# Optimization experiments

Measured on AMD Instinct MI355X. Metric: run time of the kernel, lower is better.

Reference implementation:

```python
import jax, jax.numpy as jnp
import numpy as np

MIN_PTS = 4

def setup_inputs() -> dict:
    key = jax.random.key(0)
    ks = jax.random.split(key, 10)
    P, N = 2048, 256            # proposals, max points per proposal slot
    H1, H2, OUT = 64, 128, 256  # PointNet MLP widths, extractor out_dim
    points = jax.random.normal(ks[0], (P, N, 3), dtype=jnp.float32)
    lengths = jax.random.randint(ks[1], (P,), 0, N, dtype=jnp.int32)  # some < MIN_PTS -> invalid
    centers = jax.random.normal(ks[2], (P, 3), dtype=jnp.float32) * 10.0
    sizes = jax.random.uniform(ks[3], (P, 3), minval=0.5, maxval=4.0, dtype=jnp.float32)
    proposals = jnp.concatenate([centers, sizes], axis=1)  # (P, 6)
    def lin(k, fan_in, fan_out):
        return jax.random.normal(k, (fan_in, fan_out), dtype=jnp.float32) * np.float32(1.0 / np.sqrt(fan_in))
    return {
        'points': points, 'lengths': lengths, 'proposals': proposals,
        'W1': lin(ks[4], 3, H1),   'b1': jnp.zeros((H1,), jnp.float32),
        'W2': lin(ks[5], H1, H2),  'b2': jnp.zeros((H2,), jnp.float32),
        'W3': lin(ks[6], H2, OUT), 'b3': jnp.zeros((OUT,), jnp.float32),
        'Wc': lin(ks[7], OUT, 1),  'bc': jnp.zeros((1,), jnp.float32),
        'Wr': lin(ks[8], OUT, 4),  'br': jnp.zeros((4,), jnp.float32),
    }

def reference(points, lengths, proposals, W1, b1, W2, b2, W3, b3, Wc, bc, Wr, br):
    P, N, _ = points.shape
    # repeat-padding: point i of proposal p maps to index i % n_p (gather form of the torch loop)
    L = jnp.maximum(lengths, 1)
    idx = jnp.arange(N, dtype=lengths.dtype)[None, :] % L[:, None]          # (P, N)
    batched = jnp.take_along_axis(points, idx[:, :, None], axis=1)         # (P, N, 3)
    # MultiPositionExtractor: box-normalized coords -> pointwise MLP -> max-pool
    centers = proposals[:, :3]
    half = proposals[:, 3:] * 0.5 + 1e-6
    local = (batched - centers[:, None, :]) / half[:, None, :]             # (P, N, 3)
    h = jax.nn.relu(local @ W1 + b1)                                       # (P, N, 64)
    h = jax.nn.relu(h @ W2 + b2)                                           # (P, N, 128)
    h = jax.nn.relu(h @ W3 + b3)                                           # (P, N, 256)
    feats = jnp.max(h, axis=1)                                             # (P, 256)
    # scatter-back: proposals with < MIN_PTS points get zero feature vector
    valid = lengths >= MIN_PTS
    feats = jnp.where(valid[:, None], feats, jnp.zeros((), feats.dtype))
    cls_logits = feats @ Wc + bc                                           # (P, 1)
    reg_deltas = feats @ Wr + br                                           # (P, 4)
    return cls_logits, reg_deltas
```

## Files before the change

kernel.cpp:

```cpp
#include <hip/hip_runtime.h>

#define MIN_PTS 4

typedef short bf16x8 __attribute__((ext_vector_type(8)));
typedef float f32x4  __attribute__((ext_vector_type(4)));

__device__ __forceinline__ ushort f2bf(float x) {
    unsigned u = __float_as_uint(x);
    u = (u + 0x7fffu + ((u >> 16) & 1u)) >> 16;
    return (ushort)u;
}

__global__ void pack_weights(const float* __restrict__ W2, const float* __restrict__ W3,
                             ushort* __restrict__ B2P, ushort* __restrict__ B3P)
{
    int idx = blockIdx.x * 256 + threadIdx.x;
    if (idx < 8192) {
        int j = idx & 7, l = (idx >> 3) & 63, ks = (idx >> 9) & 1, nt = idx >> 10;
        int k   = ks * 32 + (l >> 4) * 8 + j;
        int col = nt * 16 + (l & 15);
        B2P[idx] = f2bf(W2[k * 128 + col]);
    }
    if (idx < 32768) {
        int j = idx & 7, l = (idx >> 3) & 63, ks = (idx >> 9) & 3, nt = idx >> 11;
        int k   = ks * 32 + (l >> 4) * 8 + j;
        int col = nt * 16 + (l & 15);
        B3P[idx] = f2bf(W3[k * 256 + col]);
    }
}

__global__ __launch_bounds__(512, 8) void refine_stripe(
    const float* __restrict__ points,
    const int*   __restrict__ lengths,
    const float* __restrict__ proposals,
    const float* __restrict__ W1, const float* __restrict__ b1,
    const float* __restrict__ b2,
    const float* __restrict__ b3,
    const ushort* __restrict__ B2P, const ushort* __restrict__ B3P,
    int* __restrict__ featsG,
    int P, int N)
{
    const int p   = blockIdx.x;
    const int s   = blockIdx.y;
    const int len = lengths[p];
    if (len < MIN_PTS || s * 64 >= len) return;

    __shared__ __align__(16) ushort A1[4096];
    __shared__ __align__(16) ushort A3[8192];

    const int tid  = threadIdx.x;
    const int lane = tid & 63;
    const int w    = tid >> 6;
    const int rc   = lane & 15;
    const int g    = lane >> 4;

    const float cx = proposals[p * 6 + 0];
    const float cy = proposals[p * 6 + 1];
    const float cz = proposals[p * 6 + 2];
    const float rhx = __builtin_amdgcn_rcpf(fmaf(proposals[p * 6 + 3], 0.5f, 1e-6f));
    const float rhy = __builtin_amdgcn_rcpf(fmaf(proposals[p * 6 + 4], 0.5f, 1e-6f));
    const float rhz = __builtin_amdgcn_rcpf(fmaf(proposals[p * 6 + 5], 0.5f, 1e-6f));

    {
        const int jj = min(s * 64 + lane, len - 1);
        const float* pt = points + (p * N + jj) * 3;
        const float x0 = (pt[0] - cx) * rhx;
        const float x1 = (pt[1] - cy) * rhy;
        const float x2 = (pt[2] - cz) * rhz;

        union { ushort u[8]; uint4 q; } t;
        #pragma unroll
        for (int i = 0; i < 8; ++i) {
            const int f = w * 8 + i;
            float v = fmaf(x0, W1[f], fmaf(x1, W1[64 + f], fmaf(x2, W1[128 + f], b1[f])));
            t.u[i] = f2bf(fmaxf(v, 0.f));
        }
        const int mt = lane >> 4, r = lane & 15;
        const int chunk = (mt * 2 + (w >> 2)) * 64 + (w & 3) * 16 + r;
        *(uint4*)&A1[chunk * 8] = t.q;
    }
    __syncthreads();

    {
        f32x4 acc2[4];
        #pragma unroll
        for (int mt = 0; mt < 4; ++mt) acc2[mt] = (f32x4){0.f, 0.f, 0.f, 0.f};

        #pragma unroll
        for (int ks = 0; ks < 2; ++ks) {
            const bf16x8 bw = *(const bf16x8*)(B2P + ((w * 2 + ks) * 64 + lane) * 8);
            #pragma unroll
            for (int mt = 0; mt < 4; ++mt) {
                const bf16x8 a = *(const bf16x8*)&A1[((mt * 2 + ks) * 64 + lane) * 8];
                acc2[mt] = __builtin_amdgcn_mfma_f32_16x16x32_bf16(bw, a, acc2[mt], 0, 0, 0);
            }
        }
        float bias2v[4];
        #pragma unroll
        for (int rr = 0; rr < 4; ++rr) bias2v[rr] = b2[16 * w + 4 * g + rr];

        const int ks3 = w >> 1;
        const int g3  = (2 * w + (g >> 1)) & 3;
        #pragma unroll
        for (int mt = 0; mt < 4; ++mt) {
            const uint u0 = (uint)f2bf(fmaxf(acc2[mt][0] + bias2v[0], 0.f))
                          | ((uint)f2bf(fmaxf(acc2[mt][1] + bias2v[1], 0.f)) << 16);
            const uint u1 = (uint)f2bf(fmaxf(acc2[mt][2] + bias2v[2], 0.f))
                          | ((uint)f2bf(fmaxf(acc2[mt][3] + bias2v[3], 0.f)) << 16);
            const int chunk = (mt * 4 + ks3) * 64 + g3 * 16 + rc;
            uint2 val; val.x = u0; val.y = u1;
            *(uint2*)&A3[chunk * 8 + (g & 1) * 4] = val;
        }
    }
    __syncthreads();

    {
        f32x4 acc3[4][2];
        #pragma unroll
        for (int mt = 0; mt < 4; ++mt)
            #pragma unroll
            for (int j = 0; j < 2; ++j)
                acc3[mt][j] = (f32x4){0.f, 0.f, 0.f, 0.f};

        #pragma unroll
        for (int ks = 0; ks < 4; ++ks) {
            const bf16x8 bf0 = *(const bf16x8*)(B3P + (((2 * w + 0) * 4 + ks) * 64 + lane) * 8);
            const bf16x8 bf1 = *(const bf16x8*)(B3P + (((2 * w + 1) * 4 + ks) * 64 + lane) * 8);
            #pragma unroll
            for (int mt = 0; mt < 4; ++mt) {
                const bf16x8 a = *(const bf16x8*)&A3[((mt * 4 + ks) * 64 + lane) * 8];
                acc3[mt][0] = __builtin_amdgcn_mfma_f32_16x16x32_bf16(a, bf0, acc3[mt][0], 0, 0, 0);
                acc3[mt][1] = __builtin_amdgcn_mfma_f32_16x16x32_bf16(a, bf1, acc3[mt][1], 0, 0, 0);
            }
        }

        float pool[2];
        #pragma unroll
        for (int j = 0; j < 2; ++j) {
            const float b3v = b3[16 * (2 * w + j) + rc];
            float m = 0.f;
            #pragma unroll
            for (int mt = 0; mt < 4; ++mt)
                #pragma unroll
                for (int rr = 0; rr < 4; ++rr)
                    m = fmaxf(m, acc3[mt][j][rr] + b3v);
            pool[j] = m;
        }
        #pragma unroll
        for (int j = 0; j < 2; ++j) {
            pool[j] = fmaxf(pool[j], __shfl_xor(pool[j], 16, 64));
            pool[j] = fmaxf(pool[j], __shfl_xor(pool[j], 32, 64));
        }
        if (g == 0) {
            #pragma unroll
            for (int j = 0; j < 2; ++j)
                atomicMax(&featsG[p * 256 + (2 * w + j) * 16 + rc], __float_as_int(pool[j]));
        }
    }
}

__global__ __launch_bounds__(256) void heads_kernel(
    const int* __restrict__ featsG,
    const float* __restrict__ Wc, const float* __restrict__ bc,
    const float* __restrict__ Wr, const float* __restrict__ br,
    float* __restrict__ out, int P)
{
    const int tid  = threadIdx.x;
    const int lane = tid & 63;
    const int p    = blockIdx.x * 4 + (tid >> 6);
    if (p >= P) return;

    const int4 vi = *(const int4*)&featsG[p * 256 + lane * 4];
    float v[4] = {__int_as_float(vi.x), __int_as_float(vi.y),
                  __int_as_float(vi.z), __int_as_float(vi.w)};

    const float4 wc = *(const float4*)&Wc[lane * 4];
    float c  = v[0] * wc.x + v[1] * wc.y + v[2] * wc.z + v[3] * wc.w;
    float r0 = 0.f, r1 = 0.f, r2 = 0.f, r3 = 0.f;
    #pragma unroll
    for (int i = 0; i < 4; ++i) {
        const float4 wr = *(const float4*)&Wr[(lane * 4 + i) * 4];
        r0 = fmaf(v[i], wr.x, r0);
        r1 = fmaf(v[i], wr.y, r1);
        r2 = fmaf(v[i], wr.z, r2);
        r3 = fmaf(v[i], wr.w, r3);
    }
    #pragma unroll
    for (int off = 32; off > 0; off >>= 1) {
        c  += __shfl_xor(c,  off, 64);
        r0 += __shfl_xor(r0, off, 64);
        r1 += __shfl_xor(r1, off, 64);
        r2 += __shfl_xor(r2, off, 64);
        r3 += __shfl_xor(r3, off, 64);
    }
    if (lane == 0) {
        out[p]             = c  + bc[0];
        out[P + p * 4 + 0] = r0 + br[0];
        out[P + p * 4 + 1] = r1 + br[1];
        out[P + p * 4 + 2] = r2 + br[2];
        out[P + p * 4 + 3] = r3 + br[3];
    }
}

extern "C" void kernel_launch(void* const* d_in, const int* in_sizes, int n_in,
                              void* d_out, int out_size, void* d_ws, size_t ws_size,
                              hipStream_t stream)
{
    const float* points    = (const float*)d_in[0];
    const int*   lengths   = (const int*)  d_in[1];
    const float* proposals = (const float*)d_in[2];
    const float* W1 = (const float*)d_in[3];
    const float* b1 = (const float*)d_in[4];
    const float* W2 = (const float*)d_in[5];
    const float* b2 = (const float*)d_in[6];
    const float* W3 = (const float*)d_in[7];
    const float* b3 = (const float*)d_in[8];
    const float* Wc = (const float*)d_in[9];
    const float* bc = (const float*)d_in[10];
    const float* Wr = (const float*)d_in[11];
    const float* br = (const float*)d_in[12];
    float* out = (float*)d_out;

    const int P = in_sizes[1];
    const int N = in_sizes[0] / (3 * P);
    const int SMAX = (N + 63) / 64;

    ushort* B2P    = (ushort*)d_ws;
    ushort* B3P    = B2P + 8192;
    int*    featsG = (int*)((char*)d_ws + 81920);

    hipMemsetAsync(featsG, 0, (size_t)P * 256 * sizeof(int), stream);
    pack_weights<<<dim3(128), dim3(256), 0, stream>>>(W2, W3, B2P, B3P);
    refine_stripe<<<dim3(P, SMAX), dim3(512), 0, stream>>>(
        points, lengths, proposals, W1, b1, b2, b3, B2P, B3P, featsG, P, N);
    heads_kernel<<<dim3((P + 3) / 4), dim3(256), 0, stream>>>(
        featsG, Wc, bc, Wr, br, out, P);
}
```

Measured before the change: 50.04 us.

## Convert stripe kernel to persistent loop with next-item prefetch and hoisted weights

Replaces the one-block-per-(proposal, stripe) grid with a persistent grid of 2048 blocks. Each block strides over work items and prefetches the next item's length, proposal box and point while the current one computes. W1, b1, the bias vectors and the layer-2 B fragments are loaded into registers once per block, biases are folded into the accumulator init, and bf16 packing uses a packed hardware conversion. This removes per-block setup and launch cost and hides global-load latency, at the cost of more register pressure and a work index that assumes four stripes per proposal.

```diff
diff --git a/kernel.cpp b/kernel.cpp
--- a/kernel.cpp
+++ b/kernel.cpp
@@ -1,4 +1,5 @@
 #include <hip/hip_runtime.h>
+#include <hip/hip_bf16.h>
 
 #define MIN_PTS 4
 
@@ -9,6 +10,12 @@
     unsigned u = __float_as_uint(x);
     u = (u + 0x7fffu + ((u >> 16) & 1u)) >> 16;
     return (ushort)u;
+}
+
+__device__ __forceinline__ uint cvt_pk_bf16(float lo, float hi) {
+    union { __hip_bfloat162 h; uint u; } cv;
+    cv.h = __float22bfloat162_rn(make_float2(lo, hi));
+    return cv.u;
 }
 
 __global__ void pack_weights(const float* __restrict__ W2, const float* __restrict__ W3,
@@ -29,7 +36,7 @@
     }
 }
 
-__global__ __launch_bounds__(512, 8) void refine_stripe(
+__global__ __launch_bounds__(512, 8) void refine_loop(
     const float* __restrict__ points,
     const int*   __restrict__ lengths,
     const float* __restrict__ proposals,
@@ -38,124 +45,149 @@
     const float* __restrict__ b3,
     const ushort* __restrict__ B2P, const ushort* __restrict__ B3P,
     int* __restrict__ featsG,
-    int P, int N)
-{
-    const int p   = blockIdx.x;
-    const int s   = blockIdx.y;
-    const int len = lengths[p];
-    if (len < MIN_PTS || s * 64 >= len) return;
-
+    int P, int N, int work, int NB)
+{
     __shared__ __align__(16) ushort A1[4096];
     __shared__ __align__(16) ushort A3[8192];
 
     const int tid  = threadIdx.x;
     const int lane = tid & 63;
-    const int w    = tid >> 6;
+    const int wu   = __builtin_amdgcn_readfirstlane(tid >> 6);
     const int rc   = lane & 15;
     const int g    = lane >> 4;
 
-    const float cx = proposals[p * 6 + 0];
-    const float cy = proposals[p * 6 + 1];
-    const float cz = proposals[p * 6 + 2];
-    const float rhx = __builtin_amdgcn_rcpf(fmaf(proposals[p * 6 + 3], 0.5f, 1e-6f));
-    const float rhy = __builtin_amdgcn_rcpf(fmaf(proposals[p * 6 + 4], 0.5f, 1e-6f));
-    const float rhz = __builtin_amdgcn_rcpf(fmaf(proposals[p * 6 + 5], 0.5f, 1e-6f));
-
+    float w1a[8], w1b[8], w1c[8], b1r[8];
+    #pragma unroll
+    for (int i = 0; i < 8; ++i) {
+        const int f = wu * 8 + i;
+        w1a[i] = W1[f]; w1b[i] = W1[64 + f]; w1c[i] = W1[128 + f]; b1r[i] = b1[f];
+    }
+    f32x4 bias2q;
+    #pragma unroll
+    for (int rr = 0; rr < 4; ++rr) bias2q[rr] = b2[16 * wu + 4 * g + rr];
+    const float b3v0 = b3[16 * (2 * wu + 0) + rc];
+    const float b3v1 = b3[16 * (2 * wu + 1) + rc];
+    bf16x8 bw2[2];
+    #pragma unroll
+    for (int ks = 0; ks < 2; ++ks)
+        bw2[ks] = *(const bf16x8*)(B2P + ((wu * 2 + ks) * 64 + lane) * 8);
+
+    ushort* const a1wr = &A1[(((lane >> 4) * 2 + (wu >> 2)) * 64 + (wu & 3) * 16 + rc) * 8];
+    const int ks3 = wu >> 1;
+    const int g3  = (2 * wu + (g >> 1)) & 3;
+
+    int q = blockIdx.x;
+    int   lenC;
+    float cxC, cyC, czC, rxC, ryC, rzC, p0C, p1C, p2C;
     {
-        const int jj = min(s * 64 + lane, len - 1);
-        const float* pt = points + (p * N + jj) * 3;
-        const float x0 = (pt[0] - cx) * rhx;
-        const float x1 = (pt[1] - cy) * rhy;
-        const float x2 = (pt[2] - cz) * rhz;
-
-        union { ushort u[8]; uint4 q; } t;
-        #pragma unroll
-        for (int i = 0; i < 8; ++i) {
-            const int f = w * 8 + i;
-            float v = fmaf(x0, W1[f], fmaf(x1, W1[64 + f], fmaf(x2, W1[128 + f], b1[f])));
-            t.u[i] = f2bf(fmaxf(v, 0.f));
+        const int pp = q >> 2, ss = q & 3;
+        lenC = lengths[pp];
+        cxC = proposals[pp * 6 + 0]; cyC = proposals[pp * 6 + 1]; czC = proposals[pp * 6 + 2];
+        rxC = __builtin_amdgcn_rcpf(fmaf(proposals[pp * 6 + 3], 0.5f, 1e-6f));
+        ryC = __builtin_amdgcn_rcpf(fmaf(proposals[pp * 6 + 4], 0.5f, 1e-6f));
+        rzC = __builtin_amdgcn_rcpf(fmaf(proposals[pp * 6 + 5], 0.5f, 1e-6f));
+        const int jj = min(ss * 64 + lane, max(lenC, 1) - 1);
+        const float* pt = points + ((long)pp * N + jj) * 3;
+        p0C = pt[0]; p1C = pt[1]; p2C = pt[2];
+    }
+
+    while (q < work) {
+        const int   pcur = q >> 2;
+        const bool  active = (lenC >= MIN_PTS) && ((q & 3) * 64 < lenC);
+        const float cx = cxC, cy = cyC, cz = czC, rx = rxC, ry = ryC, rz = rzC;
+        const float p0 = p0C, p1 = p1C, p2 = p2C;
+
+        const int qn = q + NB;
+        if (qn < work) {
+            const int pp = qn >> 2, ss = qn & 3;
+            lenC = lengths[pp];
+            cxC = proposals[pp * 6 + 0]; cyC = proposals[pp * 6 + 1]; czC = proposals[pp * 6 + 2];
+            rxC = __builtin_amdgcn_rcpf(fmaf(proposals[pp * 6 + 3], 0.5f, 1e-6f));
+            ryC = __builtin_amdgcn_rcpf(fmaf(proposals[pp * 6 + 4], 0.5f, 1e-6f));
+            rzC = __builtin_amdgcn_rcpf(fmaf(proposals[pp * 6 + 5], 0.5f, 1e-6f));
+            const int jj = min(ss * 64 + lane, max(lenC, 1) - 1);
+            const float* pt = points + ((long)pp * N + jj) * 3;
+            p0C = pt[0]; p1C = pt[1]; p2C = pt[2];
         }
-        const int mt = lane >> 4, r = lane & 15;
-        const int chunk = (mt * 2 + (w >> 2)) * 64 + (w & 3) * 16 + r;
-        *(uint4*)&A1[chunk * 8] = t.q;
-    }
-    __syncthreads();
-
-    {
-        f32x4 acc2[4];
-        #pragma unroll
-        for (int mt = 0; mt < 4; ++mt) acc2[mt] = (f32x4){0.f, 0.f, 0.f, 0.f};
-
-        #pragma unroll
-        for (int ks = 0; ks < 2; ++ks) {
-            const bf16x8 bw = *(const bf16x8*)(B2P + ((w * 2 + ks) * 64 + lane) * 8);
-            #pragma unroll
-            for (int mt = 0; mt < 4; ++mt) {
-                const bf16x8 a = *(const bf16x8*)&A1[((mt * 2 + ks) * 64 + lane) * 8];
-                acc2[mt] = __builtin_amdgcn_mfma_f32_16x16x32_bf16(bw, a, acc2[mt], 0, 0, 0);
+
+        if (active) {
+            {
+                const float x0 = (p0 - cx) * rx;
+                const float x1 = (p1 - cy) * ry;
+                const float x2 = (p2 - cz) * rz;
+                float v[8];
+                #pragma unroll
+                for (int i = 0; i < 8; ++i)
+                    v[i] = fmaxf(fmaf(x0, w1a[i], fmaf(x1, w1b[i], fmaf(x2, w1c[i], b1r[i]))), 0.f);
+                uint4 qq;
+                qq.x = cvt_pk_bf16(v[0], v[1]);
+                qq.y = cvt_pk_bf16(v[2], v[3]);
+                qq.z = cvt_pk_bf16(v[4], v[5]);
+                qq.w = cvt_pk_bf16(v[6], v[7]);
+                *(uint4*)a1wr = qq;
+            }
+            __syncthreads();
+
+            {
+                f32x4 acc2[4];
+                #pragma unroll
+                for (int mt = 0; mt < 4; ++mt) acc2[mt] = bias2q;
+
+                #pragma unroll
+                for (int ks = 0; ks < 2; ++ks)
+                    #pragma unroll
+                    for (int mt = 0; mt < 4; ++mt) {
+                        const bf16x8 a = *(const bf16x8*)&A1[((mt * 2 + ks) * 64 + lane) * 8];
+                        acc2[mt] = __builtin_amdgcn_mfma_f32_16x16x32_bf16(bw2[ks], a, acc2[mt], 0, 0, 0);
+                    }
+                #pragma unroll
+                for (int mt = 0; mt < 4; ++mt) {
+                    const uint u0 = cvt_pk_bf16(fmaxf(acc2[mt][0], 0.f), fmaxf(acc2[mt][1], 0.f));
+                    const uint u1 = cvt_pk_bf16(fmaxf(acc2[mt][2], 0.f), fmaxf(acc2[mt][3], 0.f));
+                    const int chunk = (mt * 4 + ks3) * 64 + g3 * 16 + rc;
+                    uint2 val; val.x = u0; val.y = u1;
+                    *(uint2*)&A3[chunk * 8 + (g & 1) * 4] = val;
+                }
+            }
+            __syncthreads();
+
+            {
+                f32x4 acc3a[4], acc3b[4];
+                #pragma unroll
+                for (int mt = 0; mt < 4; ++mt) {
+                    acc3a[mt] = (f32x4){b3v0, b3v0, b3v0, b3v0};
+                    acc3b[mt] = (f32x4){b3v1, b3v1, b3v1, b3v1};
+                }
+                #pragma unroll
+                for (int ks = 0; ks < 4; ++ks) {
+                    const bf16x8 bf0 = *(const bf16x8*)(B3P + (((2 * wu + 0) * 4 + ks) * 64 + lane) * 8);
+                    const bf16x8 bf1 = *(const bf16x8*)(B3P + (((2 * wu + 1) * 4 + ks) * 64 + lane) * 8);
+                    #pragma unroll
+                    for (int mt = 0; mt < 4; ++mt) {
+                        const bf16x8 a = *(const bf16x8*)&A3[((mt * 4 + ks) * 64 + lane) * 8];
+                        acc3a[mt] = __builtin_amdgcn_mfma_f32_16x16x32_bf16(a, bf0, acc3a[mt], 0, 0, 0);
+                        acc3b[mt] = __builtin_amdgcn_mfma_f32_16x16x32_bf16(a, bf1, acc3b[mt], 0, 0, 0);
+                    }
+                }
+                float pool0 = 0.f, pool1 = 0.f;
+                #pragma unroll
+                for (int mt = 0; mt < 4; ++mt)
+                    #pragma unroll
+                    for (int rr = 0; rr < 4; ++rr) {
+                        pool0 = fmaxf(pool0, acc3a[mt][rr]);
+                        pool1 = fmaxf(pool1, acc3b[mt][rr]);
+                    }
+                pool0 = fmaxf(pool0, __shfl_xor(pool0, 16, 64));
+                pool0 = fmaxf(pool0, __shfl_xor(pool0, 32, 64));
+                pool1 = fmaxf(pool1, __shfl_xor(pool1, 16, 64));
+                pool1 = fmaxf(pool1, __shfl_xor(pool1, 32, 64));
+                if (g == 0) {
+                    atomicMax(&featsG[pcur * 256 + (2 * wu + 0) * 16 + rc], __float_as_int(pool0));
+                    atomicMax(&featsG[pcur * 256 + (2 * wu + 1) * 16 + rc], __float_as_int(pool1));
+                }
             }
         }
-        float bias2v[4];
-        #pragma unroll
-        for (int rr = 0; rr < 4; ++rr) bias2v[rr] = b2[16 * w + 4 * g + rr];
-
-        const int ks3 = w >> 1;
-        const int g3  = (2 * w + (g >> 1)) & 3;
-        #pragma unroll
-        for (int mt = 0; mt < 4; ++mt) {
-            const uint u0 = (uint)f2bf(fmaxf(acc2[mt][0] + bias2v[0], 0.f))
-                          | ((uint)f2bf(fmaxf(acc2[mt][1] + bias2v[1], 0.f)) << 16);
-            const uint u1 = (uint)f2bf(fmaxf(acc2[mt][2] + bias2v[2], 0.f))
-                          | ((uint)f2bf(fmaxf(acc2[mt][3] + bias2v[3], 0.f)) << 16);
-            const int chunk = (mt * 4 + ks3) * 64 + g3 * 16 + rc;
-            uint2 val; val.x = u0; val.y = u1;
-            *(uint2*)&A3[chunk * 8 + (g & 1) * 4] = val;
-        }
-    }
-    __syncthreads();
-
-    {
-        f32x4 acc3[4][2];
-        #pragma unroll
-        for (int mt = 0; mt < 4; ++mt)
-            #pragma unroll
-            for (int j = 0; j < 2; ++j)
-                acc3[mt][j] = (f32x4){0.f, 0.f, 0.f, 0.f};
-
-        #pragma unroll
-        for (int ks = 0; ks < 4; ++ks) {
-            const bf16x8 bf0 = *(const bf16x8*)(B3P + (((2 * w + 0) * 4 + ks) * 64 + lane) * 8);
-            const bf16x8 bf1 = *(const bf16x8*)(B3P + (((2 * w + 1) * 4 + ks) * 64 + lane) * 8);
-            #pragma unroll
-            for (int mt = 0; mt < 4; ++mt) {
-                const bf16x8 a = *(const bf16x8*)&A3[((mt * 4 + ks) * 64 + lane) * 8];
-                acc3[mt][0] = __builtin_amdgcn_mfma_f32_16x16x32_bf16(a, bf0, acc3[mt][0], 0, 0, 0);
-                acc3[mt][1] = __builtin_amdgcn_mfma_f32_16x16x32_bf16(a, bf1, acc3[mt][1], 0, 0, 0);
-            }
-        }
-
-        float pool[2];
-        #pragma unroll
-        for (int j = 0; j < 2; ++j) {
-            const float b3v = b3[16 * (2 * w + j) + rc];
-            float m = 0.f;
-            #pragma unroll
-            for (int mt = 0; mt < 4; ++mt)
-                #pragma unroll
-                for (int rr = 0; rr < 4; ++rr)
-                    m = fmaxf(m, acc3[mt][j][rr] + b3v);
-            pool[j] = m;
-        }
-        #pragma unroll
-        for (int j = 0; j < 2; ++j) {
-            pool[j] = fmaxf(pool[j], __shfl_xor(pool[j], 16, 64));
-            pool[j] = fmaxf(pool[j], __shfl_xor(pool[j], 32, 64));
-        }
-        if (g == 0) {
-            #pragma unroll
-            for (int j = 0; j < 2; ++j)
-                atomicMax(&featsG[p * 256 + (2 * w + j) * 16 + rc], __float_as_int(pool[j]));
-        }
+        q = qn;
     }
 }
 
@@ -224,6 +256,8 @@
     const int P = in_sizes[1];
     const int N = in_sizes[0] / (3 * P);
     const int SMAX = (N + 63) / 64;
+    const int work = P * SMAX;
+    const int NB   = 2048;
 
     ushort* B2P    = (ushort*)d_ws;
     ushort* B3P    = B2P + 8192;
@@ -231,8 +265,9 @@
 
     hipMemsetAsync(featsG, 0, (size_t)P * 256 * sizeof(int), stream);
     pack_weights<<<dim3(128), dim3(256), 0, stream>>>(W2, W3, B2P, B3P);
-    refine_stripe<<<dim3(P, SMAX), dim3(512), 0, stream>>>(
-        points, lengths, proposals, W1, b1, b2, b3, B2P, B3P, featsG, P, N);
+    refine_loop<<<dim3(NB), dim3(512), 0, stream>>>(
+        points, lengths, proposals, W1, b1, b2, b3, B2P, B3P, featsG,
+        P, N, work, NB);
     heads_kernel<<<dim3((P + 3) / 4), dim3(256), 0, stream>>>(
         featsG, Wc, bc, Wr, br, out, P);
 }
```

Result: slower. 109.4 us (+118.6%).

## Shrink stripes to 32 points with 4-wave blocks and packed bf16 conversion

Applied to the files above, without the earlier changes.

Each block now handles 32 points with 256 threads instead of 64 points with 512, on a flattened 1D grid. Because point counts vary per proposal, finer stripes cut the padded work done beyond each proposal's length. Each wave now covers more output columns per layer. The layer-3 pass loops over two column halves to keep register use low. Biases are folded into the accumulator initial values, bf16 packing uses the hardware paired conversion, and W1 is read with vector loads. The trade-off is twice as many blocks, each reusing weights over fewer points, plus more atomics per proposal. The flattened grid hardcodes 8 stripes per proposal (bid>>3) and is only correct when N is 256.

```diff
diff --git a/kernel.cpp b/kernel.cpp
--- a/kernel.cpp
+++ b/kernel.cpp
@@ -1,4 +1,5 @@
 #include <hip/hip_runtime.h>
+#include <hip/hip_bf16.h>
 
 #define MIN_PTS 4
 
@@ -9,6 +10,12 @@
     unsigned u = __float_as_uint(x);
     u = (u + 0x7fffu + ((u >> 16) & 1u)) >> 16;
     return (ushort)u;
+}
+
+__device__ __forceinline__ uint cvt_pk_bf16(float lo, float hi) {
+    union { __hip_bfloat162 h; uint u; } cv;
+    cv.h = __float22bfloat162_rn(make_float2(lo, hi));
+    return cv.u;
 }
 
 __global__ void pack_weights(const float* __restrict__ W2, const float* __restrict__ W3,
@@ -29,7 +36,7 @@
     }
 }
 
-__global__ __launch_bounds__(512, 8) void refine_stripe(
+__global__ __launch_bounds__(256, 8) void refine_stripe32(
     const float* __restrict__ points,
     const int*   __restrict__ lengths,
     const float* __restrict__ proposals,
@@ -40,121 +47,135 @@
     int* __restrict__ featsG,
     int P, int N)
 {
-    const int p   = blockIdx.x;
-    const int s   = blockIdx.y;
+    const int bid = blockIdx.x;
+    const int p   = bid >> 3;
+    const int s   = bid & 7;
     const int len = lengths[p];
-    if (len < MIN_PTS || s * 64 >= len) return;
-
-    __shared__ __align__(16) ushort A1[4096];
-    __shared__ __align__(16) ushort A3[8192];
+    if (len < MIN_PTS || s * 32 >= len) return;
+
+    __shared__ __align__(16) ushort A1[2048];
+    __shared__ __align__(16) ushort A3[4096];
 
     const int tid  = threadIdx.x;
     const int lane = tid & 63;
-    const int w    = tid >> 6;
+    const int wu   = __builtin_amdgcn_readfirstlane(tid >> 6);
     const int rc   = lane & 15;
     const int g    = lane >> 4;
+    const int h    = lane >> 5;
+    const int ptl  = lane & 31;
+    const int mtA  = (lane >> 4) & 1;
 
     const float cx = proposals[p * 6 + 0];
     const float cy = proposals[p * 6 + 1];
     const float cz = proposals[p * 6 + 2];
-    const float rhx = __builtin_amdgcn_rcpf(fmaf(proposals[p * 6 + 3], 0.5f, 1e-6f));
-    const float rhy = __builtin_amdgcn_rcpf(fmaf(proposals[p * 6 + 4], 0.5f, 1e-6f));
-    const float rhz = __builtin_amdgcn_rcpf(fmaf(proposals[p * 6 + 5], 0.5f, 1e-6f));
+    const float rx = __builtin_amdgcn_rcpf(fmaf(proposals[p * 6 + 3], 0.5f, 1e-6f));
+    const float ry = __builtin_amdgcn_rcpf(fmaf(proposals[p * 6 + 4], 0.5f, 1e-6f));
+    const float rz = __builtin_amdgcn_rcpf(fmaf(proposals[p * 6 + 5], 0.5f, 1e-6f));
 
     {
-        const int jj = min(s * 64 + lane, len - 1);
-        const float* pt = points + (p * N + jj) * 3;
-        const float x0 = (pt[0] - cx) * rhx;
-        const float x1 = (pt[1] - cy) * rhy;
-        const float x2 = (pt[2] - cz) * rhz;
-
-        union { ushort u[8]; uint4 q; } t;
-        #pragma unroll
-        for (int i = 0; i < 8; ++i) {
-            const int f = w * 8 + i;
-            float v = fmaf(x0, W1[f], fmaf(x1, W1[64 + f], fmaf(x2, W1[128 + f], b1[f])));
-            t.u[i] = f2bf(fmaxf(v, 0.f));
-        }
-        const int mt = lane >> 4, r = lane & 15;
-        const int chunk = (mt * 2 + (w >> 2)) * 64 + (w & 3) * 16 + r;
-        *(uint4*)&A1[chunk * 8] = t.q;
+        const int jj = min(s * 32 + ptl, len - 1);
+        const float* pt = points + ((long)p * N + jj) * 3;
+        const float x0 = (pt[0] - cx) * rx;
+        const float x1 = (pt[1] - cy) * ry;
+        const float x2 = (pt[2] - cz) * rz;
+
+        const int f0 = 16 * wu + 8 * h;
+        const float4 wa0 = *(const float4*)&W1[f0],       wa1 = *(const float4*)&W1[f0 + 4];
+        const float4 wb0 = *(const float4*)&W1[64 + f0],  wb1 = *(const float4*)&W1[64 + f0 + 4];
+        const float4 wc0 = *(const float4*)&W1[128 + f0], wc1 = *(const float4*)&W1[128 + f0 + 4];
+        const float4 bb0 = *(const float4*)&b1[f0],       bb1 = *(const float4*)&b1[f0 + 4];
+
+        float v[8];
+        v[0] = fmaxf(fmaf(x0, wa0.x, fmaf(x1, wb0.x, fmaf(x2, wc0.x, bb0.x))), 0.f);
+        v[1] = fmaxf(fmaf(x0, wa0.y, fmaf(x1, wb0.y, fmaf(x2, wc0.y, bb0.y))), 0.f);
+        v[2] = fmaxf(fmaf(x0, wa0.z, fmaf(x1, wb0.z, fmaf(x2, wc0.z, bb0.z))), 0.f);
+        v[3] = fmaxf(fmaf(x0, wa0.w, fmaf(x1, wb0.w, fmaf(x2, wc0.w, bb0.w))), 0.f);
+        v[4] = fmaxf(fmaf(x0, wa1.x, fmaf(x1, wb1.x, fmaf(x2, wc1.x, bb1.x))), 0.f);
+        v[5] = fmaxf(fmaf(x0, wa1.y, fmaf(x1, wb1.y, fmaf(x2, wc1.y, bb1.y))), 0.f);
+        v[6] = fmaxf(fmaf(x0, wa1.z, fmaf(x1, wb1.z, fmaf(x2, wc1.z, bb1.z))), 0.f);
+        v[7] = fmaxf(fmaf(x0, wa1.w, fmaf(x1, wb1.w, fmaf(x2, wc1.w, bb1.w))), 0.f);
+
+        uint4 qq;
+        qq.x = cvt_pk_bf16(v[0], v[1]);
+        qq.y = cvt_pk_bf16(v[2], v[3]);
+        qq.z = cvt_pk_bf16(v[4], v[5]);
+        qq.w = cvt_pk_bf16(v[6], v[7]);
+        const int chunk = (mtA * 2 + (wu >> 1)) * 64 + ((2 * wu + h) & 3) * 16 + rc;
+        *(uint4*)&A1[chunk * 8] = qq;
     }
     __syncthreads();
 
     {
-        f32x4 acc2[4];
-        #pragma unroll
-        for (int mt = 0; mt < 4; ++mt) acc2[mt] = (f32x4){0.f, 0.f, 0.f, 0.f};
-
+        f32x4 acc2[2][2];
+        #pragma unroll
+        for (int nt = 0; nt < 2; ++nt) {
+            f32x4 bq;
+            #pragma unroll
+            for (int rr = 0; rr < 4; ++rr) bq[rr] = b2[32 * wu + 16 * nt + 4 * g + rr];
+            acc2[0][nt] = bq; acc2[1][nt] = bq;
+        }
         #pragma unroll
         for (int ks = 0; ks < 2; ++ks) {
-            const bf16x8 bw = *(const bf16x8*)(B2P + ((w * 2 + ks) * 64 + lane) * 8);
-            #pragma unroll
-            for (int mt = 0; mt < 4; ++mt) {
+            const bf16x8 bw0 = *(const bf16x8*)(B2P + (((2 * wu + 0) * 2 + ks) * 64 + lane) * 8);
+            const bf16x8 bw1 = *(const bf16x8*)(B2P + (((2 * wu + 1) * 2 + ks) * 64 + lane) * 8);
+            #pragma unroll
+            for (int mt = 0; mt < 2; ++mt) {
                 const bf16x8 a = *(const bf16x8*)&A1[((mt * 2 + ks) * 64 + lane) * 8];
-                acc2[mt] = __builtin_amdgcn_mfma_f32_16x16x32_bf16(bw, a, acc2[mt], 0, 0, 0);
-            }
-        }
-        float bias2v[4];
-        #pragma unroll
-        for (int rr = 0; rr < 4; ++rr) bias2v[rr] = b2[16 * w + 4 * g + rr];
-
-        const int ks3 = w >> 1;
-        const int g3  = (2 * w + (g >> 1)) & 3;
-        #pragma unroll
-        for (int mt = 0; mt < 4; ++mt) {
-            const uint u0 = (uint)f2bf(fmaxf(acc2[mt][0] + bias2v[0], 0.f))
-                          | ((uint)f2bf(fmaxf(acc2[mt][1] + bias2v[1], 0.f)) << 16);
-            const uint u1 = (uint)f2bf(fmaxf(acc2[mt][2] + bias2v[2], 0.f))
-                          | ((uint)f2bf(fmaxf(acc2[mt][3] + bias2v[3], 0.f)) << 16);
-            const int chunk = (mt * 4 + ks3) * 64 + g3 * 16 + rc;
-            uint2 val; val.x = u0; val.y = u1;
-            *(uint2*)&A3[chunk * 8 + (g & 1) * 4] = val;
-        }
+                acc2[mt][0] = __builtin_amdgcn_mfma_f32_16x16x32_bf16(bw0, a, acc2[mt][0], 0, 0, 0);
+                acc2[mt][1] = __builtin_amdgcn_mfma_f32_16x16x32_bf16(bw1, a, acc2[mt][1], 0, 0, 0);
+            }
+        }
+        #pragma unroll
+        for (int mt = 0; mt < 2; ++mt)
+            #pragma unroll
+            for (int nt = 0; nt < 2; ++nt) {
+                const uint u0 = cvt_pk_bf16(fmaxf(acc2[mt][nt][0], 0.f), fmaxf(acc2[mt][nt][1], 0.f));
+                const uint u1 = cvt_pk_bf16(fmaxf(acc2[mt][nt][2], 0.f), fmaxf(acc2[mt][nt][3], 0.f));
+                const int g3 = (2 * nt + (g >> 1)) & 3;
+                const int chunk = (mt * 4 + wu) * 64 + g3 * 16 + rc;
+                uint2 val; val.x = u0; val.y = u1;
+                *(uint2*)&A3[chunk * 8 + (g & 1) * 4] = val;
+            }
     }
     __syncthreads();
 
-    {
-        f32x4 acc3[4][2];
-        #pragma unroll
-        for (int mt = 0; mt < 4; ++mt)
-            #pragma unroll
-            for (int j = 0; j < 2; ++j)
-                acc3[mt][j] = (f32x4){0.f, 0.f, 0.f, 0.f};
-
+    #pragma unroll 1
+    for (int nh = 0; nh < 2; ++nh) {
+        const int nt0 = 4 * wu + 2 * nh, nt1 = nt0 + 1;
+        const float b30 = b3[16 * nt0 + rc];
+        const float b31 = b3[16 * nt1 + rc];
+        f32x4 acc[2][2];
+        #pragma unroll
+        for (int mt = 0; mt < 2; ++mt) {
+            acc[mt][0] = (f32x4){b30, b30, b30, b30};
+            acc[mt][1] = (f32x4){b31, b31, b31, b31};
+        }
         #pragma unroll
         for (int ks = 0; ks < 4; ++ks) {
-            const bf16x8 bf0 = *(const bf16x8*)(B3P + (((2 * w + 0) * 4 + ks) * 64 + lane) * 8);
-            const bf16x8 bf1 = *(const bf16x8*)(B3P + (((2 * w + 1) * 4 + ks) * 64 + lane) * 8);
-            #pragma unroll
-            for (int mt = 0; mt < 4; ++mt) {
+            const bf16x8 bf0 = *(const bf16x8*)(B3P + ((nt0 * 4 + ks) * 64 + lane) * 8);
+            const bf16x8 bf1 = *(const bf16x8*)(B3P + ((nt1 * 4 + ks) * 64 + lane) * 8);
+            #pragma unroll
+            for (int mt = 0; mt < 2; ++mt) {
                 const bf16x8 a = *(const bf16x8*)&A3[((mt * 4 + ks) * 64 + lane) * 8];
-                acc3[mt][0] = __builtin_amdgcn_mfma_f32_16x16x32_bf16(a, bf0, acc3[mt][0], 0, 0, 0);
-                acc3[mt][1] = __builtin_amdgcn_mfma_f32_16x16x32_bf16(a, bf1, acc3[mt][1], 0, 0, 0);
-            }
-        }
-
-        float pool[2];
-        #pragma unroll
-        for (int j = 0; j < 2; ++j) {
-            const float b3v = b3[16 * (2 * w + j) + rc];
-            float m = 0.f;
-            #pragma unroll
-            for (int mt = 0; mt < 4; ++mt)
-                #pragma unroll
-                for (int rr = 0; rr < 4; ++rr)
-                    m = fmaxf(m, acc3[mt][j][rr] + b3v);
-            pool[j] = m;
-        }
-        #pragma unroll
-        for (int j = 0; j < 2; ++j) {
-            pool[j] = fmaxf(pool[j], __shfl_xor(pool[j], 16, 64));
-            pool[j] = fmaxf(pool[j], __shfl_xor(pool[j], 32, 64));
-        }
+                acc[mt][0] = __builtin_amdgcn_mfma_f32_16x16x32_bf16(a, bf0, acc[mt][0], 0, 0, 0);
+                acc[mt][1] = __builtin_amdgcn_mfma_f32_16x16x32_bf16(a, bf1, acc[mt][1], 0, 0, 0);
+            }
+        }
+        float pool0 = 0.f, pool1 = 0.f;
+        #pragma unroll
+        for (int mt = 0; mt < 2; ++mt)
+            #pragma unroll
+            for (int rr = 0; rr < 4; ++rr) {
+                pool0 = fmaxf(pool0, acc[mt][0][rr]);
+                pool1 = fmaxf(pool1, acc[mt][1][rr]);
+            }
+        pool0 = fmaxf(pool0, __shfl_xor(pool0, 16, 64));
+        pool0 = fmaxf(pool0, __shfl_xor(pool0, 32, 64));
+        pool1 = fmaxf(pool1, __shfl_xor(pool1, 16, 64));
+        pool1 = fmaxf(pool1, __shfl_xor(pool1, 32, 64));
         if (g == 0) {
-            #pragma unroll
-            for (int j = 0; j < 2; ++j)
-                atomicMax(&featsG[p * 256 + (2 * w + j) * 16 + rc], __float_as_int(pool[j]));
+            atomicMax(&featsG[p * 256 + nt0 * 16 + rc], __float_as_int(pool0));
+            atomicMax(&featsG[p * 256 + nt1 * 16 + rc], __float_as_int(pool1));
         }
     }
 }
@@ -223,7 +244,7 @@
 
     const int P = in_sizes[1];
     const int N = in_sizes[0] / (3 * P);
-    const int SMAX = (N + 63) / 64;
+    const int S32 = (N + 31) / 32;
 
     ushort* B2P    = (ushort*)d_ws;
     ushort* B3P    = B2P + 8192;
@@ -231,7 +252,7 @@
 
     hipMemsetAsync(featsG, 0, (size_t)P * 256 * sizeof(int), stream);
     pack_weights<<<dim3(128), dim3(256), 0, stream>>>(W2, W3, B2P, B3P);
-    refine_stripe<<<dim3(P, SMAX), dim3(512), 0, stream>>>(
+    refine_stripe32<<<dim3(P * S32), dim3(256), 0, stream>>>(
         points, lengths, proposals, W1, b1, b2, b3, B2P, B3P, featsG, P, N);
     heads_kernel<<<dim3((P + 3) / 4), dim3(256), 0, stream>>>(
         featsG, Wc, bc, Wr, br, out, P);
```

Result: slower. 84.94 us (+69.7%).
